# Optimization experiments

Hardware: AMD Instinct MI355X
Metric: run time of the kernel (lower is better)

The kernel has to match this reference:

```python
import jax, jax.numpy as jnp
import numpy as np

N, K, C, D4, HID, HEAD, DEPTH = 40000, 16, 128, 32, 512, 256, 4
EPS = 1e-5  # BatchNorm eps; eval mode with running_mean=0, running_var=1


def _bn(x, g, b):
    # eval-mode BatchNorm1d with fresh running stats (mean=0, var=1)
    return x * (g / np.sqrt(1.0 + EPS)) + b


def _mlp(x, w1, b1, w2, g, b):
    # Linear -> GELU -> Linear(no bias) -> BN
    return _bn(jax.nn.gelu(x @ w1 + b1) @ w2, g, b)


def _lfp(x, lxyz, knn, proj, coor, scale, g, b):
    # LFP: Linear(no bias) -> la_spse_a4 (neighbor gather + anisotropic spatial
    # positional encoding, one PE channel per 4 feature channels, max-pool over k) -> BN
    xp = x @ proj                                   # (N, C)
    xn = xp[knn]                                    # (N, K, C) irregular gather
    rel3 = (lxyz[knn] - lxyz[:, None])[..., :3]     # (N, K, 3)
    pe = jnp.einsum('nkc,cd->nkd', rel3, coor) * jnp.square(scale)  # (N, K, D4)
    out = jnp.max(xn.reshape(N, K, D4, 4) + pe[..., None], axis=1).reshape(N, C)
    return _bn(out, g, b)


def _knn_spse4(lxyz, feat, knn, m_sp, c, h):
    # knn_spse_4: squared anisotropic spatial distances (3 learned 4-d directions
    # per output channel, 12 params) + per-channel color (3) + height (1) weighted
    # squared diffs, averaged over k neighbors; caller takes sqrt.
    rel4 = lxyz[knn] - lxyz[:, None]                # (N, K, 4)
    relf = feat[knn] - feat[:, None]                # (N, K, 4) = color(3)+height(1)
    dirs = m_sp.reshape(3, 4, C)
    e = jnp.zeros((N, K, C), jnp.float32)
    for j in range(3):  # fixed small loop over 3 learned directions
        e = e + jnp.square(jnp.einsum('nkc,cd->nkd', rel4, dirs[j]))
    e = e + jnp.einsum('nki,id->nkd', jnp.square(relf[..., :3]), jnp.square(c))
    e = e + jnp.square(relf[..., 3:4]) * jnp.square(h)
    return jnp.sqrt(e.mean(axis=1))                 # (N, C)


def setup_inputs():
    key = jax.random.key(0)
    ks = jax.random.split(key, 32)
    rn = lambda i, s, sc=0.02: jax.random.normal(ks[i], s, jnp.float32) * sc
    gm = lambda i, s: 1.0 + jax.random.normal(ks[i], s, jnp.float32) * 0.1
    return {
        'x': rn(0, (N, 4), 1.0),
        'xyz': jax.random.uniform(ks[1], (N, 3), jnp.float32),
        'knn': jax.random.randint(ks[2], (N, K), 0, N, jnp.int32),
        'spse_m': rn(3, (12, C), 0.5),
        'spse_c': rn(4, (3, C), 0.5),
        'spse_h': rn(5, (C,), 0.5),
        'nbr_bn0_g': gm(6, (C,)), 'nbr_bn0_b': rn(7, (C,)),
        'nbr_w1': rn(8, (C, 2 * C)), 'nbr_b1': rn(9, (2 * C,)),
        'nbr_w2': rn(10, (2 * C, C)),
        'nbr_bn_g': gm(11, (C,)), 'nbr_bn_b': rn(12, (C,)),
        'lfp_proj': rn(13, (DEPTH, C, C)),
        'lfp_coor': rn(14, (DEPTH, 3, D4), 0.5),
        'lfp_scale': 0.1 + rn(15, (DEPTH, D4), 0.01),
        'lfp_bng': gm(16, (DEPTH, C)), 'lfp_bnb': rn(17, (DEPTH, C)),
        'mlp_w1': rn(18, (3, C, HID)), 'mlp_b1': rn(19, (3, HID)),
        'mlp_w2': rn(20, (3, HID, C)),
        'mlp_bng': gm(21, (3, C)), 'mlp_bnb': rn(22, (3, C)),
        'post_bn_g': gm(23, (C,)), 'post_bn_b': rn(24, (C,)),
        'post_w': rn(25, (C, HEAD)),
    }


def reference(x, xyz, knn, spse_m, spse_c, spse_h, nbr_bn0_g, nbr_bn0_b,
              nbr_w1, nbr_b1, nbr_w2, nbr_bn_g, nbr_bn_b,
              lfp_proj, lfp_coor, lfp_scale, lfp_bng, lfp_bnb,
              mlp_w1, mlp_b1, mlp_w2, mlp_bng, mlp_bnb,
              post_bn_g, post_bn_b, post_w):
    # Stage.forward, first==last stage, eval mode (no drop_path, no closs).
    lxyz = jnp.pad(xyz, ((0, 0), (0, 1)))  # cor_std = 1.0
    nbr = _knn_spse4(lxyz, x, knn, spse_m, spse_c, spse_h)
    nbr = _bn(nbr, nbr_bn0_g, nbr_bn0_b)
    nbr = jax.nn.gelu(nbr @ nbr_w1 + nbr_b1) @ nbr_w2   # nbr_proj
    h = _bn(nbr, nbr_bn_g, nbr_bn_b)                    # nbr_bn; x = nbr (first stage)
    # Block: residual MLP, then DEPTH LFPs with an MLP after every 2nd LFP
    h = h + _mlp(h, mlp_w1[0], mlp_b1[0], mlp_w2[0], mlp_bng[0], mlp_bnb[0])
    for i in range(DEPTH):
        h = h + _lfp(h, lxyz, knn, lfp_proj[i], lfp_coor[i], lfp_scale[i],
                     lfp_bng[i], lfp_bnb[i])
        if i % 2 == 1:
            j = i // 2 + 1
            h = h + _mlp(h, mlp_w1[j], mlp_b1[j], mlp_w2[j], mlp_bng[j], mlp_bnb[j])
    return _bn(h, post_bn_g, post_bn_b) @ post_w        # postproj -> (N, HEAD)
```

## Files before the change

kernel.cpp:

```cpp
#include <hip/hip_runtime.h>
#include <hip/hip_bf16.h>
#include <math.h>

#define NPTS 40000
#define KNB 16
#define CH 128

typedef unsigned short u16;
typedef __attribute__((ext_vector_type(8))) short bf16x8;
typedef __attribute__((ext_vector_type(4))) float f32x4;

__device__ __forceinline__ float gelu_f(float v) {
  const float u = 0.7978845608028654f * (v + 0.044715f * v * v * v);
  const float t = __builtin_amdgcn_exp2f(-2.8853900817779268f * u);
  return v * __builtin_amdgcn_rcpf(1.0f + t);
}

__device__ __forceinline__ float bnscale(float g) {
  return g * rsqrtf(1.0f + 1e-5f);
}

__device__ __forceinline__ u16 f2bf(float x) {
  union { __hip_bfloat16 b; u16 u; } cv;
  cv.b = __float2bfloat16(x);
  return cv.u;
}

__device__ __forceinline__ float bf2f(u16 u) {
  union { float f; unsigned int i; } cv;
  cv.i = ((unsigned int)u) << 16;
  return cv.f;
}

__device__ __forceinline__ void bf16split(float x, u16& hi, u16& lo) {
  hi = f2bf(x);
  lo = f2bf(x - bf2f(hi));
}

__device__ __forceinline__ void gl2lds(const u16* gp, u16* lp) {
  __builtin_amdgcn_global_load_lds(
      (const __attribute__((address_space(1))) void*)gp,
      (__attribute__((address_space(3))) void*)lp, 16, 0, 0);
}

__global__ __launch_bounds__(128) void spse_kernel(
    const float* __restrict__ x, const float* __restrict__ xyz,
    const int* __restrict__ knn, const float* __restrict__ sm,
    const float* __restrict__ sc, const float* __restrict__ sh,
    const float* __restrict__ g0, const float* __restrict__ b0,
    u16* __restrict__ oh, u16* __restrict__ ol) {
  const int n = blockIdx.x;
  const int c = threadIdx.x;
  __shared__ float sr[KNB][3];
  __shared__ float sf[KNB][4];
  if (c < KNB) {
    const int j = knn[n * KNB + c];
    sr[c][0] = xyz[j * 3 + 0] - xyz[n * 3 + 0];
    sr[c][1] = xyz[j * 3 + 1] - xyz[n * 3 + 1];
    sr[c][2] = xyz[j * 3 + 2] - xyz[n * 3 + 2];
    float f0 = x[j * 4 + 0] - x[n * 4 + 0];
    float f1 = x[j * 4 + 1] - x[n * 4 + 1];
    float f2 = x[j * 4 + 2] - x[n * 4 + 2];
    float f3 = x[j * 4 + 3] - x[n * 4 + 3];
    sf[c][0] = f0 * f0; sf[c][1] = f1 * f1;
    sf[c][2] = f2 * f2; sf[c][3] = f3 * f3;
  }
  __syncthreads();
  const float m0 = sm[c], m1 = sm[CH + c], m2 = sm[2 * CH + c];
  const float m4 = sm[4 * CH + c], m5 = sm[5 * CH + c], m6 = sm[6 * CH + c];
  const float m8 = sm[8 * CH + c], m9 = sm[9 * CH + c], m10 = sm[10 * CH + c];
  float c0 = sc[c];          c0 *= c0;
  float c1 = sc[CH + c];     c1 *= c1;
  float c2 = sc[2 * CH + c]; c2 *= c2;
  float h2 = sh[c];          h2 *= h2;
  float e = 0.0f;
#pragma unroll
  for (int k = 0; k < KNB; k++) {
    const float r0 = sr[k][0], r1 = sr[k][1], r2 = sr[k][2];
    const float d0 = fmaf(r2, m2, fmaf(r1, m1, r0 * m0));
    const float d1 = fmaf(r2, m6, fmaf(r1, m5, r0 * m4));
    const float d2 = fmaf(r2, m10, fmaf(r1, m9, r0 * m8));
    e = fmaf(d0, d0, e);
    e = fmaf(d1, d1, e);
    e = fmaf(d2, d2, e);
    e = fmaf(sf[k][0], c0, e);
    e = fmaf(sf[k][1], c1, e);
    e = fmaf(sf[k][2], c2, e);
    e = fmaf(sf[k][3], h2, e);
  }
  const float v = sqrtf(e * (1.0f / KNB)) * bnscale(g0[c]) + b0[c];
  u16 hi, lo; bf16split(v, hi, lo);
  const size_t idx = (size_t)n * CH + c;
  oh[idx] = hi; ol[idx] = lo;
}

__global__ __launch_bounds__(256) void lfp_kernel(
    const u16* __restrict__ xp, const int* __restrict__ knn,
    const float* __restrict__ xyz, const float* __restrict__ coor,
    const float* __restrict__ scale, const float* __restrict__ g,
    const float* __restrict__ b, u16* __restrict__ hh, u16* __restrict__ hl) {
  const int t = threadIdx.x;
  const int bid = blockIdx.x;
  __shared__ int si[16][KNB];
  __shared__ float sr[16][KNB][3];
  {
    const int pp = t >> 4, kk = t & 15;
    const int n = bid * 16 + pp;
    const int j = knn[n * KNB + kk];
    si[pp][kk] = j;
    sr[pp][kk][0] = xyz[j * 3 + 0] - xyz[n * 3 + 0];
    sr[pp][kk][1] = xyz[j * 3 + 1] - xyz[n * 3 + 1];
    sr[pp][kk][2] = xyz[j * 3 + 2] - xyz[n * 3 + 2];
  }
  __syncthreads();
  const int p = t >> 4, d8 = t & 15;
  const int n = bid * 16 + p;
  const float c0a = coor[d8 * 2],     c1a = coor[32 + d8 * 2],     c2a = coor[64 + d8 * 2];
  const float c0b = coor[d8 * 2 + 1], c1b = coor[32 + d8 * 2 + 1], c2b = coor[64 + d8 * 2 + 1];
  float s2a = scale[d8 * 2];     s2a *= s2a;
  float s2b = scale[d8 * 2 + 1]; s2b *= s2b;
  float a[8];
#pragma unroll
  for (int e = 0; e < 8; e++) a[e] = -3.0e38f;
#pragma unroll
  for (int k = 0; k < KNB; k++) {
    const int j = si[p][k];
    const float r0 = sr[p][k][0], r1 = sr[p][k][1], r2 = sr[p][k][2];
    const float pea = fmaf(r2, c2a, fmaf(r1, c1a, r0 * c0a)) * s2a;
    const float peb = fmaf(r2, c2b, fmaf(r1, c1b, r0 * c0b)) * s2b;
    const bf16x8 v = *(const bf16x8*)(xp + (size_t)j * CH + d8 * 8);
#pragma unroll
    for (int e = 0; e < 4; e++) a[e] = fmaxf(a[e], bf2f((u16)v[e]) + pea);
#pragma unroll
    for (int e = 4; e < 8; e++) a[e] = fmaxf(a[e], bf2f((u16)v[e]) + peb);
  }
  const size_t off = (size_t)n * CH + d8 * 8;
  union { u16 a[8]; uint4 v; } ih, il, oh, ol;
  ih.v = *(const uint4*)(hh + off);
  il.v = *(const uint4*)(hl + off);
#pragma unroll
  for (int e = 0; e < 8; e++) {
    const int c = d8 * 8 + e;
    const float nv = bf2f(ih.a[e]) + bf2f(il.a[e]) + a[e] * bnscale(g[c]) + b[c];
    u16 hi, lo; bf16split(nv, hi, lo);
    oh.a[e] = hi; ol.a[e] = lo;
  }
  *(uint4*)(hh + off) = oh.v;
  *(uint4*)(hl + off) = ol.v;
}

__global__ __launch_bounds__(256) void prep_weights(
    const float* __restrict__ nw1, const float* __restrict__ nw2,
    const float* __restrict__ mw1, const float* __restrict__ mw2,
    const float* __restrict__ lproj, const float* __restrict__ pw,
    const float* __restrict__ pg, u16* __restrict__ th, u16* __restrict__ tl) {
  const int idx = blockIdx.x * 256 + threadIdx.x;
  const float* src;
  int local, Kd, Nd, dst, swz;
  float scale = 1.0f;
  if (idx < 32768)        { src = nw1; local = idx;          Kd = 128; Nd = 256; dst = 0; swz = 0; }
  else if (idx < 65536)   { src = nw2; local = idx - 32768;  Kd = 256; Nd = 128; dst = 32768; swz = 1; }
  else if (idx < 262144)  { int j = (idx - 65536) >> 16;  local = (idx - 65536) & 65535;
                            src = mw1 + j * 65536; Kd = 128; Nd = 512; dst = 65536 + j * 65536; swz = 0; }
  else if (idx < 458752)  { int j = (idx - 262144) >> 16; local = (idx - 262144) & 65535;
                            src = mw2 + j * 65536; Kd = 512; Nd = 128; dst = 262144 + j * 65536; swz = 1; }
  else if (idx < 524288)  { int i = (idx - 458752) >> 14; local = (idx - 458752) & 16383;
                            src = lproj + i * 16384; Kd = 128; Nd = 128; dst = 458752 + i * 16384; swz = 0; }
  else if (idx < 557056)  { local = idx - 524288; src = pw; Kd = 128; Nd = 256; dst = 524288; swz = 0;
                            scale = bnscale(pg[local >> 8]); }
  else return;
  const int k = local / Nd, n = local % Nd;
  const float v = src[local] * scale;
  u16 hi, lo; bf16split(v, hi, lo);
  const int ks = swz ? ((k & ~63) | ((k & 63) ^ ((n & 7) << 3))) : k;
  const int o = dst + n * Kd + ks;
  th[o] = hi; tl[o] = lo;
}

__global__ __launch_bounds__(256) void fold_pb(const float* __restrict__ pw,
                                               const float* __restrict__ pb,
                                               float* __restrict__ fb) {
  const int t = threadIdx.x;
  float a = 0.0f;
  for (int k = 0; k < 128; k++) a = fmaf(pb[k], pw[k * 256 + t], a);
  fb[t] = a;
}

template <int EPI>
__global__ __launch_bounds__(256, 2) void k128_reg(
    const u16* __restrict__ Ahi, const u16* __restrict__ Alo,
    const u16* __restrict__ Wth, const u16* __restrict__ Wtl,
    const float* __restrict__ p0, u16* __restrict__ outu,
    float* __restrict__ outf, int ostride, int ntiles) {
  const int t = threadIdx.x, lane = t & 63, w = t >> 6;
  const int col0 = blockIdx.y * 128;
  const int wm0 = (w >> 1) * 32, wn0 = (w & 1) * 64;
  const int lc = lane & 15, lq = lane >> 4;
  const int lq8 = lq * 8, lq4 = lq * 4;

  bf16x8 wh[4][4], wl[4][4];
  float bv[4];
#pragma unroll
  for (int nf = 0; nf < 4; nf++) {
    const int nr = col0 + wn0 + nf * 16 + lc;
    const u16* wr = Wth + (size_t)nr * 128;
    const u16* wr2 = Wtl + (size_t)nr * 128;
#pragma unroll
    for (int ks = 0; ks < 4; ks++) {
      wh[nf][ks] = *(const bf16x8*)(wr + ks * 32 + lq8);
      wl[nf][ks] = *(const bf16x8*)(wr2 + ks * 32 + lq8);
    }
    bv[nf] = (EPI == 0) ? 0.0f : p0[nr];
  }

  const f32x4 zz = {0.0f, 0.0f, 0.0f, 0.0f};
  for (int tile = blockIdx.x; tile < ntiles; tile += gridDim.x) {
    const int row0 = tile * 64;
    f32x4 acc[2][4];
#pragma unroll
    for (int mf = 0; mf < 2; mf++)
#pragma unroll
      for (int nf = 0; nf < 4; nf++) acc[mf][nf] = zz;
#pragma unroll
    for (int ks = 0; ks < 4; ks++) {
      bf16x8 ah[2], al[2];
#pragma unroll
      for (int mf = 0; mf < 2; mf++) {
        const size_t ao = (size_t)(row0 + wm0 + mf * 16 + lc) * 128 + ks * 32 + lq8;
        ah[mf] = *(const bf16x8*)(Ahi + ao);
        al[mf] = *(const bf16x8*)(Alo + ao);
      }
#pragma unroll
      for (int mf = 0; mf < 2; mf++)
#pragma unroll
        for (int nf = 0; nf < 4; nf++) {
          acc[mf][nf] = __builtin_amdgcn_mfma_f32_16x16x32_bf16(ah[mf], wh[nf][ks], acc[mf][nf], 0, 0, 0);
          acc[mf][nf] = __builtin_amdgcn_mfma_f32_16x16x32_bf16(ah[mf], wl[nf][ks], acc[mf][nf], 0, 0, 0);
          acc[mf][nf] = __builtin_amdgcn_mfma_f32_16x16x32_bf16(al[mf], wh[nf][ks], acc[mf][nf], 0, 0, 0);
        }
    }
#pragma unroll
    for (int mf = 0; mf < 2; mf++)
#pragma unroll
      for (int q = 0; q < 4; q++) {
        const int r = row0 + wm0 + mf * 16 + lq4 + q;
#pragma unroll
        for (int nf = 0; nf < 4; nf++) {
          const int col = col0 + wn0 + nf * 16 + lc;
          const size_t off = (size_t)r * ostride + col;
          const float v = acc[mf][nf][q];
          if (EPI == 0)      outu[off] = f2bf(v);
          else if (EPI == 1) outu[off] = f2bf(gelu_f(v + bv[nf]));
          else               outf[off] = v + bv[nf];
        }
      }
  }
}

template <int K, bool RES>
__global__ __launch_bounds__(256, 3) void gemm_w2(
    const u16* __restrict__ A, const u16* __restrict__ Wth,
    const u16* __restrict__ Wtl, const float* __restrict__ g,
    const float* __restrict__ bb, u16* __restrict__ hh, u16* __restrict__ hl) {
  __shared__ __align__(16) u16 Ws[2][128 * 64];
  const int t = threadIdx.x, lane = t & 63, w = t >> 6;
  const int row0 = blockIdx.x * 64;
  const int wm0 = (w >> 1) * 32, wn0 = (w & 1) * 64;
  const int lc = lane & 15, lq = lane >> 4;
  const int lq8 = lq * 8, lq4 = lq * 4;

  const f32x4 zz = {0.0f, 0.0f, 0.0f, 0.0f};
  f32x4 acc[2][4];
#pragma unroll
  for (int mf = 0; mf < 2; mf++)
#pragma unroll
    for (int nf = 0; nf < 4; nf++) acc[mf][nf] = zz;

  auto stage_slab = [&](u16* lds, int kb) {
#pragma unroll
    for (int i = 0; i < 1024; i += 256) {
      const int wc0 = i + w * 64;
      const int c = wc0 + lane;
      gl2lds(Wth + (size_t)(c >> 3) * K + kb + (c & 7) * 8, lds + wc0 * 8);
    }
  };
  auto load_af = [&](bf16x8 (&dst)[2][2], int kb) {
#pragma unroll
    for (int mf = 0; mf < 2; mf++)
#pragma unroll
      for (int ks = 0; ks < 2; ks++)
        dst[mf][ks] = *(const bf16x8*)(A + (size_t)(row0 + wm0 + mf * 16 + lc) * K +
                                       kb + ks * 32 + lq8);
  };

  bf16x8 afc[2][2], afn[2][2];
  stage_slab(Ws[0], 0);
  load_af(afc, 0);
  __syncthreads();

  constexpr int NT = K / 64;
#pragma unroll 2
  for (int tt = 0; tt < NT; tt++) {
    const int cur = tt & 1;
    if (tt + 1 < NT) {
      stage_slab(Ws[cur ^ 1], (tt + 1) * 64);
      load_af(afn, (tt + 1) * 64);
    }
#pragma unroll
    for (int ks = 0; ks < 2; ks++) {
      bf16x8 whf[4], wlf[4];
#pragma unroll
      for (int nf = 0; nf < 4; nf++) {
        const int nr = wn0 + nf * 16 + lc;
        const int j = (ks * 32 + lq8) ^ ((nr & 7) << 3);
        whf[nf] = *(const bf16x8*)(Ws[cur] + nr * 64 + j);
        wlf[nf] = *(const bf16x8*)(Wtl + (size_t)nr * K + tt * 64 + j);
      }
#pragma unroll
      for (int mf = 0; mf < 2; mf++)
#pragma unroll
        for (int nf = 0; nf < 4; nf++) {
          acc[mf][nf] = __builtin_amdgcn_mfma_f32_16x16x32_bf16(afc[mf][ks], whf[nf], acc[mf][nf], 0, 0, 0);
          acc[mf][nf] = __builtin_amdgcn_mfma_f32_16x16x32_bf16(afc[mf][ks], wlf[nf], acc[mf][nf], 0, 0, 0);
        }
    }
    __syncthreads();
#pragma unroll
    for (int mf = 0; mf < 2; mf++)
#pragma unroll
      for (int ks = 0; ks < 2; ks++) afc[mf][ks] = afn[mf][ks];
  }

  float S0[4], S1[4];
#pragma unroll
  for (int nf = 0; nf < 4; nf++) {
    const int col = wn0 + nf * 16 + lc;
    S0[nf] = bnscale(g[col]);
    S1[nf] = bb[col];
  }
#pragma unroll
  for (int mf = 0; mf < 2; mf++)
#pragma unroll
    for (int q = 0; q < 4; q++) {
      const int r = row0 + wm0 + mf * 16 + lq4 + q;
#pragma unroll
      for (int nf = 0; nf < 4; nf++) {
        const int col = wn0 + nf * 16 + lc;
        const size_t off = (size_t)r * CH + col;
        float v = acc[mf][nf][q] * S0[nf] + S1[nf];
        if (RES) v += bf2f(hh[off]) + bf2f(hl[off]);
        u16 hi, lo; bf16split(v, hi, lo);
        hh[off] = hi; hl[off] = lo;
      }
    }
}

extern "C" void kernel_launch(void* const* d_in, const int* in_sizes, int n_in,
                              void* d_out, int out_size, void* d_ws, size_t ws_size,
                              hipStream_t stream) {
  const float* x    = (const float*)d_in[0];
  const float* xyz  = (const float*)d_in[1];
  const int*   knn  = (const int*)d_in[2];
  const float* sm   = (const float*)d_in[3];
  const float* scc  = (const float*)d_in[4];
  const float* shh  = (const float*)d_in[5];
  const float* bn0g = (const float*)d_in[6];
  const float* bn0b = (const float*)d_in[7];
  const float* nw1  = (const float*)d_in[8];
  const float* nb1  = (const float*)d_in[9];
  const float* nw2  = (const float*)d_in[10];
  const float* nbng = (const float*)d_in[11];
  const float* nbnb = (const float*)d_in[12];
  const float* lproj  = (const float*)d_in[13];
  const float* lcoor  = (const float*)d_in[14];
  const float* lscale = (const float*)d_in[15];
  const float* lbng   = (const float*)d_in[16];
  const float* lbnb   = (const float*)d_in[17];
  const float* mw1  = (const float*)d_in[18];
  const float* mb1  = (const float*)d_in[19];
  const float* mw2  = (const float*)d_in[20];
  const float* mbng = (const float*)d_in[21];
  const float* mbnb = (const float*)d_in[22];
  const float* pg   = (const float*)d_in[23];
  const float* pb   = (const float*)d_in[24];
  const float* pw   = (const float*)d_in[25];
  float* out = (float*)d_out;

  char* ws = (char*)d_ws;
  u16*   h_hi = (u16*)(ws + 0);
  u16*   h_lo = (u16*)(ws + 10240000);
  u16*   act  = (u16*)(ws + 20480000);
  u16*   xp   = (u16*)(ws + 20480000);
  u16*   Wh   = (u16*)(ws + 61440000);
  u16*   Wl   = (u16*)(ws + 62554112);
  float* fb   = (float*)(ws + 63668224);

  const u16* nw1t   = Wh + 0;
  const u16* nw2t   = Wh + 32768;
  const u16* mw1t   = Wh + 65536;
  const u16* mw2t   = Wh + 262144;
  const u16* lprojt = Wh + 458752;
  const u16* postt  = Wh + 524288;
  const u16* nw1tl   = Wl + 0;
  const u16* nw2tl   = Wl + 32768;
  const u16* mw1tl   = Wl + 65536;
  const u16* mw2tl   = Wl + 262144;
  const u16* lprojtl = Wl + 458752;
  const u16* posttl  = Wl + 524288;

  prep_weights<<<2176, 256, 0, stream>>>(nw1, nw2, mw1, mw2, lproj, pw, pg, Wh, Wl);
  fold_pb<<<1, 256, 0, stream>>>(pw, pb, fb);

  spse_kernel<<<NPTS, 128, 0, stream>>>(x, xyz, knn, sm, scc, shh, bn0g, bn0b, h_hi, h_lo);

  k128_reg<1><<<dim3(256, 2), 256, 0, stream>>>(h_hi, h_lo, nw1t, nw1tl, nb1,
                                                act, nullptr, 256, 625);
  gemm_w2<256, false><<<625, 256, 0, stream>>>(act, nw2t, nw2tl, nbng, nbnb, h_hi, h_lo);

  k128_reg<1><<<dim3(128, 4), 256, 0, stream>>>(h_hi, h_lo, mw1t, mw1tl, mb1,
                                                act, nullptr, 512, 625);
  gemm_w2<512, true><<<625, 256, 0, stream>>>(act, mw2t, mw2tl, mbng, mbnb, h_hi, h_lo);

  for (int i = 0; i < 4; i++) {
    k128_reg<0><<<dim3(625, 1), 256, 0, stream>>>(h_hi, h_lo, lprojt + i * 16384,
                                                  lprojtl + i * 16384, nullptr,
                                                  xp, nullptr, 128, 625);
    lfp_kernel<<<2500, 256, 0, stream>>>(xp, knn, xyz, lcoor + i * 96, lscale + i * 32,
                                         lbng + i * 128, lbnb + i * 128, h_hi, h_lo);
    if (i & 1) {
      const int j = i / 2 + 1;
      k128_reg<1><<<dim3(128, 4), 256, 0, stream>>>(h_hi, h_lo, mw1t + j * 65536,
                                                    mw1tl + j * 65536, mb1 + j * 512,
                                                    act, nullptr, 512, 625);
      gemm_w2<512, true><<<625, 256, 0, stream>>>(act, mw2t + j * 65536, mw2tl + j * 65536,
                                                  mbng + j * 128, mbnb + j * 128,
                                                  h_hi, h_lo);
    }
  }

  k128_reg<2><<<dim3(256, 2), 256, 0, stream>>>(h_hi, h_lo, postt, posttl, fb,
                                                nullptr, out, 256, 625);
}
```

Before: 497.2 us.

## Fuse MLP up- and down-projection GEMMs through LDS-resident hidden activations

Replaces the separate W1 GEMM (GELU epilogue writing a bf16 hidden buffer to global memory) and W2 GEMM with one kernel per MLP. Each 512-thread block computes a 64-row tile of the hidden activation, keeps it in a swizzled LDS buffer, then runs the second GEMM from LDS with the BN and residual epilogue. This removes the global write and read of the large (N x 512) intermediate and halves the launch count. In exchange, weights are read straight from global memory without LDS staging or double buffering. The 64 KB LDS footprint also allows only one block per CU, which limits latency hiding.

```diff
diff --git a/kernel.cpp b/kernel.cpp
--- a/kernel.cpp
+++ b/kernel.cpp
@@ -35,12 +35,6 @@
 __device__ __forceinline__ void bf16split(float x, u16& hi, u16& lo) {
   hi = f2bf(x);
   lo = f2bf(x - bf2f(hi));
-}
-
-__device__ __forceinline__ void gl2lds(const u16* gp, u16* lp) {
-  __builtin_amdgcn_global_load_lds(
-      (const __attribute__((address_space(1))) void*)gp,
-      (__attribute__((address_space(3))) void*)lp, 16, 0, 0);
 }
 
 __global__ __launch_bounds__(128) void spse_kernel(
@@ -156,24 +150,23 @@
     const float* __restrict__ pg, u16* __restrict__ th, u16* __restrict__ tl) {
   const int idx = blockIdx.x * 256 + threadIdx.x;
   const float* src;
-  int local, Kd, Nd, dst, swz;
+  int local, Kd, Nd, dst;
   float scale = 1.0f;
-  if (idx < 32768)        { src = nw1; local = idx;          Kd = 128; Nd = 256; dst = 0; swz = 0; }
-  else if (idx < 65536)   { src = nw2; local = idx - 32768;  Kd = 256; Nd = 128; dst = 32768; swz = 1; }
+  if (idx < 32768)        { src = nw1; local = idx;          Kd = 128; Nd = 256; dst = 0; }
+  else if (idx < 65536)   { src = nw2; local = idx - 32768;  Kd = 256; Nd = 128; dst = 32768; }
   else if (idx < 262144)  { int j = (idx - 65536) >> 16;  local = (idx - 65536) & 65535;
-                            src = mw1 + j * 65536; Kd = 128; Nd = 512; dst = 65536 + j * 65536; swz = 0; }
+                            src = mw1 + j * 65536; Kd = 128; Nd = 512; dst = 65536 + j * 65536; }
   else if (idx < 458752)  { int j = (idx - 262144) >> 16; local = (idx - 262144) & 65535;
-                            src = mw2 + j * 65536; Kd = 512; Nd = 128; dst = 262144 + j * 65536; swz = 1; }
+                            src = mw2 + j * 65536; Kd = 512; Nd = 128; dst = 262144 + j * 65536; }
   else if (idx < 524288)  { int i = (idx - 458752) >> 14; local = (idx - 458752) & 16383;
-                            src = lproj + i * 16384; Kd = 128; Nd = 128; dst = 458752 + i * 16384; swz = 0; }
-  else if (idx < 557056)  { local = idx - 524288; src = pw; Kd = 128; Nd = 256; dst = 524288; swz = 0;
+                            src = lproj + i * 16384; Kd = 128; Nd = 128; dst = 458752 + i * 16384; }
+  else if (idx < 557056)  { local = idx - 524288; src = pw; Kd = 128; Nd = 256; dst = 524288;
                             scale = bnscale(pg[local >> 8]); }
   else return;
   const int k = local / Nd, n = local % Nd;
   const float v = src[local] * scale;
   u16 hi, lo; bf16split(v, hi, lo);
-  const int ks = swz ? ((k & ~63) | ((k & 63) ^ ((n & 7) << 3))) : k;
-  const int o = dst + n * Kd + ks;
+  const int o = dst + n * Kd + k;
   th[o] = hi; tl[o] = lo;
 }
 
@@ -249,92 +242,115 @@
           const int col = col0 + wn0 + nf * 16 + lc;
           const size_t off = (size_t)r * ostride + col;
           const float v = acc[mf][nf][q];
-          if (EPI == 0)      outu[off] = f2bf(v);
-          else if (EPI == 1) outu[off] = f2bf(gelu_f(v + bv[nf]));
-          else               outf[off] = v + bv[nf];
+          if (EPI == 0) outu[off] = f2bf(v);
+          else          outf[off] = v + bv[nf];
         }
       }
   }
 }
 
-template <int K, bool RES>
-__global__ __launch_bounds__(256, 3) void gemm_w2(
-    const u16* __restrict__ A, const u16* __restrict__ Wth,
-    const u16* __restrict__ Wtl, const float* __restrict__ g,
+template <int HID, bool RES>
+__global__ __launch_bounds__(512, 1) void mlp_fused(
+    const u16* __restrict__ Ahi, const u16* __restrict__ Alo,
+    const u16* __restrict__ W1t, const u16* __restrict__ W1tl,
+    const u16* __restrict__ W2t, const u16* __restrict__ W2tl,
+    const float* __restrict__ b1, const float* __restrict__ g,
     const float* __restrict__ bb, u16* __restrict__ hh, u16* __restrict__ hl) {
-  __shared__ __align__(16) u16 Ws[2][128 * 64];
+  constexpr int HID8 = HID / 8;
+  constexpr int NF1 = HID8 / 16;
+  constexpr int NKS2 = HID / 32;
+  __shared__ __align__(16) u16 act[64 * HID];
   const int t = threadIdx.x, lane = t & 63, w = t >> 6;
   const int row0 = blockIdx.x * 64;
-  const int wm0 = (w >> 1) * 32, wn0 = (w & 1) * 64;
   const int lc = lane & 15, lq = lane >> 4;
   const int lq8 = lq * 8, lq4 = lq * 4;
+  const int cw0 = w * HID8;
 
   const f32x4 zz = {0.0f, 0.0f, 0.0f, 0.0f};
-  f32x4 acc[2][4];
+  f32x4 acc1[4][NF1];
+#pragma unroll
+  for (int mf = 0; mf < 4; mf++)
+#pragma unroll
+    for (int nf = 0; nf < NF1; nf++) acc1[mf][nf] = zz;
+
+#pragma unroll
+  for (int ks = 0; ks < 4; ks++) {
+    bf16x8 ah[4], al[4];
+#pragma unroll
+    for (int mf = 0; mf < 4; mf++) {
+      const size_t ao = (size_t)(row0 + mf * 16 + lc) * 128 + ks * 32 + lq8;
+      ah[mf] = *(const bf16x8*)(Ahi + ao);
+      al[mf] = *(const bf16x8*)(Alo + ao);
+    }
+    bf16x8 w1h[NF1], w1l[NF1];
+#pragma unroll
+    for (int nf = 0; nf < NF1; nf++) {
+      const size_t wo = (size_t)(cw0 + nf * 16 + lc) * 128 + ks * 32 + lq8;
+      w1h[nf] = *(const bf16x8*)(W1t + wo);
+      w1l[nf] = *(const bf16x8*)(W1tl + wo);
+    }
+#pragma unroll
+    for (int mf = 0; mf < 4; mf++)
+#pragma unroll
+      for (int nf = 0; nf < NF1; nf++) {
+        acc1[mf][nf] = __builtin_amdgcn_mfma_f32_16x16x32_bf16(ah[mf], w1h[nf], acc1[mf][nf], 0, 0, 0);
+        acc1[mf][nf] = __builtin_amdgcn_mfma_f32_16x16x32_bf16(ah[mf], w1l[nf], acc1[mf][nf], 0, 0, 0);
+        acc1[mf][nf] = __builtin_amdgcn_mfma_f32_16x16x32_bf16(al[mf], w1h[nf], acc1[mf][nf], 0, 0, 0);
+      }
+  }
+  float b1v[NF1];
+#pragma unroll
+  for (int nf = 0; nf < NF1; nf++) b1v[nf] = b1[cw0 + nf * 16 + lc];
+#pragma unroll
+  for (int mf = 0; mf < 4; mf++)
+#pragma unroll
+    for (int nf = 0; nf < NF1; nf++)
+#pragma unroll
+      for (int q = 0; q < 4; q++) {
+        const int row = mf * 16 + lq4 + q;
+        const int col = cw0 + nf * 16 + lc;
+        const int cs = (col & ~63) | ((col & 63) ^ ((row & 7) << 3));
+        act[row * HID + cs] = f2bf(gelu_f(acc1[mf][nf][q] + b1v[nf]));
+      }
+  __syncthreads();
+
+  const int wr = w >> 2, wc = w & 3;
+  f32x4 acc[2][2];
 #pragma unroll
   for (int mf = 0; mf < 2; mf++)
 #pragma unroll
-    for (int nf = 0; nf < 4; nf++) acc[mf][nf] = zz;
-
-  auto stage_slab = [&](u16* lds, int kb) {
-#pragma unroll
-    for (int i = 0; i < 1024; i += 256) {
-      const int wc0 = i + w * 64;
-      const int c = wc0 + lane;
-      gl2lds(Wth + (size_t)(c >> 3) * K + kb + (c & 7) * 8, lds + wc0 * 8);
-    }
-  };
-  auto load_af = [&](bf16x8 (&dst)[2][2], int kb) {
+    for (int nf = 0; nf < 2; nf++) acc[mf][nf] = zz;
+
+#pragma unroll
+  for (int ks = 0; ks < NKS2; ks++) {
+    bf16x8 af[2];
+#pragma unroll
+    for (int mf = 0; mf < 2; mf++) {
+      const int r = wr * 32 + mf * 16 + lc;
+      const int cb = ks * 32 + lq8;
+      const int cs = (cb & ~63) | ((cb & 63) ^ ((r & 7) << 3));
+      af[mf] = *(const bf16x8*)(act + r * HID + cs);
+    }
+    bf16x8 w2h[2], w2l[2];
+#pragma unroll
+    for (int nf = 0; nf < 2; nf++) {
+      const size_t wo = (size_t)(wc * 32 + nf * 16 + lc) * HID + ks * 32 + lq8;
+      w2h[nf] = *(const bf16x8*)(W2t + wo);
+      w2l[nf] = *(const bf16x8*)(W2tl + wo);
+    }
 #pragma unroll
     for (int mf = 0; mf < 2; mf++)
 #pragma unroll
-      for (int ks = 0; ks < 2; ks++)
-        dst[mf][ks] = *(const bf16x8*)(A + (size_t)(row0 + wm0 + mf * 16 + lc) * K +
-                                       kb + ks * 32 + lq8);
-  };
-
-  bf16x8 afc[2][2], afn[2][2];
-  stage_slab(Ws[0], 0);
-  load_af(afc, 0);
-  __syncthreads();
-
-  constexpr int NT = K / 64;
-#pragma unroll 2
-  for (int tt = 0; tt < NT; tt++) {
-    const int cur = tt & 1;
-    if (tt + 1 < NT) {
-      stage_slab(Ws[cur ^ 1], (tt + 1) * 64);
-      load_af(afn, (tt + 1) * 64);
-    }
-#pragma unroll
-    for (int ks = 0; ks < 2; ks++) {
-      bf16x8 whf[4], wlf[4];
-#pragma unroll
-      for (int nf = 0; nf < 4; nf++) {
-        const int nr = wn0 + nf * 16 + lc;
-        const int j = (ks * 32 + lq8) ^ ((nr & 7) << 3);
-        whf[nf] = *(const bf16x8*)(Ws[cur] + nr * 64 + j);
-        wlf[nf] = *(const bf16x8*)(Wtl + (size_t)nr * K + tt * 64 + j);
-      }
-#pragma unroll
-      for (int mf = 0; mf < 2; mf++)
-#pragma unroll
-        for (int nf = 0; nf < 4; nf++) {
-          acc[mf][nf] = __builtin_amdgcn_mfma_f32_16x16x32_bf16(afc[mf][ks], whf[nf], acc[mf][nf], 0, 0, 0);
-          acc[mf][nf] = __builtin_amdgcn_mfma_f32_16x16x32_bf16(afc[mf][ks], wlf[nf], acc[mf][nf], 0, 0, 0);
-        }
-    }
-    __syncthreads();
-#pragma unroll
-    for (int mf = 0; mf < 2; mf++)
-#pragma unroll
-      for (int ks = 0; ks < 2; ks++) afc[mf][ks] = afn[mf][ks];
-  }
-
-  float S0[4], S1[4];
-#pragma unroll
-  for (int nf = 0; nf < 4; nf++) {
-    const int col = wn0 + nf * 16 + lc;
+      for (int nf = 0; nf < 2; nf++) {
+        acc[mf][nf] = __builtin_amdgcn_mfma_f32_16x16x32_bf16(af[mf], w2h[nf], acc[mf][nf], 0, 0, 0);
+        acc[mf][nf] = __builtin_amdgcn_mfma_f32_16x16x32_bf16(af[mf], w2l[nf], acc[mf][nf], 0, 0, 0);
+      }
+  }
+
+  float S0[2], S1[2];
+#pragma unroll
+  for (int nf = 0; nf < 2; nf++) {
+    const int col = wc * 32 + nf * 16 + lc;
     S0[nf] = bnscale(g[col]);
     S1[nf] = bb[col];
   }
@@ -342,10 +358,10 @@
   for (int mf = 0; mf < 2; mf++)
 #pragma unroll
     for (int q = 0; q < 4; q++) {
-      const int r = row0 + wm0 + mf * 16 + lq4 + q;
-#pragma unroll
-      for (int nf = 0; nf < 4; nf++) {
-        const int col = wn0 + nf * 16 + lc;
+      const int r = row0 + wr * 32 + mf * 16 + lq4 + q;
+#pragma unroll
+      for (int nf = 0; nf < 2; nf++) {
+        const int col = wc * 32 + nf * 16 + lc;
         const size_t off = (size_t)r * CH + col;
         float v = acc[mf][nf][q] * S0[nf] + S1[nf];
         if (RES) v += bf2f(hh[off]) + bf2f(hl[off]);
@@ -389,7 +405,6 @@
   char* ws = (char*)d_ws;
   u16*   h_hi = (u16*)(ws + 0);
   u16*   h_lo = (u16*)(ws + 10240000);
-  u16*   act  = (u16*)(ws + 20480000);
   u16*   xp   = (u16*)(ws + 20480000);
   u16*   Wh   = (u16*)(ws + 61440000);
   u16*   Wl   = (u16*)(ws + 62554112);
@@ -413,13 +428,10 @@
 
   spse_kernel<<<NPTS, 128, 0, stream>>>(x, xyz, knn, sm, scc, shh, bn0g, bn0b, h_hi, h_lo);
 
-  k128_reg<1><<<dim3(256, 2), 256, 0, stream>>>(h_hi, h_lo, nw1t, nw1tl, nb1,
-                                                act, nullptr, 256, 625);
-  gemm_w2<256, false><<<625, 256, 0, stream>>>(act, nw2t, nw2tl, nbng, nbnb, h_hi, h_lo);
-
-  k128_reg<1><<<dim3(128, 4), 256, 0, stream>>>(h_hi, h_lo, mw1t, mw1tl, mb1,
-                                                act, nullptr, 512, 625);
-  gemm_w2<512, true><<<625, 256, 0, stream>>>(act, mw2t, mw2tl, mbng, mbnb, h_hi, h_lo);
+  mlp_fused<256, false><<<625, 512, 0, stream>>>(
+      h_hi, h_lo, nw1t, nw1tl, nw2t, nw2tl, nb1, nbng, nbnb, h_hi, h_lo);
+  mlp_fused<512, true><<<625, 512, 0, stream>>>(
+      h_hi, h_lo, mw1t, mw1tl, mw2t, mw2tl, mb1, mbng, mbnb, h_hi, h_lo);
 
   for (int i = 0; i < 4; i++) {
     k128_reg<0><<<dim3(625, 1), 256, 0, stream>>>(h_hi, h_lo, lprojt + i * 16384,
@@ -429,12 +441,9 @@
                                          lbng + i * 128, lbnb + i * 128, h_hi, h_lo);
     if (i & 1) {
       const int j = i / 2 + 1;
-      k128_reg<1><<<dim3(128, 4), 256, 0, stream>>>(h_hi, h_lo, mw1t + j * 65536,
-                                                    mw1tl + j * 65536, mb1 + j * 512,
-                                                    act, nullptr, 512, 625);
-      gemm_w2<512, true><<<625, 256, 0, stream>>>(act, mw2t + j * 65536, mw2tl + j * 65536,
-                                                  mbng + j * 128, mbnb + j * 128,
-                                                  h_hi, h_lo);
+      mlp_fused<512, true><<<625, 512, 0, stream>>>(
+          h_hi, h_lo, mw1t + j * 65536, mw1tl + j * 65536, mw2t + j * 65536,
+          mw2tl + j * 65536, mb1 + j * 512, mbng + j * 128, mbnb + j * 128, h_hi, h_lo);
     }
   }
 
```

New measurement: 619.9 us. 24.7% more time.

## Drop activation-low split in hidden GEMMs and simplify W2 GEMM to direct global loads

Applied to the files above, without the earlier changes.

The k128_reg GEMMs gain an NSPLIT template parameter. Every layer except the final post-projection drops the activation-low term, so each of those GEMMs issues 2 MFMAs per fragment instead of 3 and skips loading the Alo tile. The gemm_w2 kernel loses its LDS double-buffered weight staging and swizzle and now reads the weight hi and lo fragments straight from global memory, with occupancy bound lowered from 3 to 2. This cuts matrix-core work and removes LDS and sync overhead, at the cost of lower precision in the hidden layers and more global or L2 traffic for weights.

```diff
diff --git a/kernel.cpp b/kernel.cpp
--- a/kernel.cpp
+++ b/kernel.cpp
@@ -35,12 +35,6 @@
 __device__ __forceinline__ void bf16split(float x, u16& hi, u16& lo) {
   hi = f2bf(x);
   lo = f2bf(x - bf2f(hi));
-}
-
-__device__ __forceinline__ void gl2lds(const u16* gp, u16* lp) {
-  __builtin_amdgcn_global_load_lds(
-      (const __attribute__((address_space(1))) void*)gp,
-      (__attribute__((address_space(3))) void*)lp, 16, 0, 0);
 }
 
 __global__ __launch_bounds__(128) void spse_kernel(
@@ -156,24 +150,23 @@
     const float* __restrict__ pg, u16* __restrict__ th, u16* __restrict__ tl) {
   const int idx = blockIdx.x * 256 + threadIdx.x;
   const float* src;
-  int local, Kd, Nd, dst, swz;
+  int local, Kd, Nd, dst;
   float scale = 1.0f;
-  if (idx < 32768)        { src = nw1; local = idx;          Kd = 128; Nd = 256; dst = 0; swz = 0; }
-  else if (idx < 65536)   { src = nw2; local = idx - 32768;  Kd = 256; Nd = 128; dst = 32768; swz = 1; }
+  if (idx < 32768)        { src = nw1; local = idx;          Kd = 128; Nd = 256; dst = 0; }
+  else if (idx < 65536)   { src = nw2; local = idx - 32768;  Kd = 256; Nd = 128; dst = 32768; }
   else if (idx < 262144)  { int j = (idx - 65536) >> 16;  local = (idx - 65536) & 65535;
-                            src = mw1 + j * 65536; Kd = 128; Nd = 512; dst = 65536 + j * 65536; swz = 0; }
+                            src = mw1 + j * 65536; Kd = 128; Nd = 512; dst = 65536 + j * 65536; }
   else if (idx < 458752)  { int j = (idx - 262144) >> 16; local = (idx - 262144) & 65535;
-                            src = mw2 + j * 65536; Kd = 512; Nd = 128; dst = 262144 + j * 65536; swz = 1; }
+                            src = mw2 + j * 65536; Kd = 512; Nd = 128; dst = 262144 + j * 65536; }
   else if (idx < 524288)  { int i = (idx - 458752) >> 14; local = (idx - 458752) & 16383;
-                            src = lproj + i * 16384; Kd = 128; Nd = 128; dst = 458752 + i * 16384; swz = 0; }
-  else if (idx < 557056)  { local = idx - 524288; src = pw; Kd = 128; Nd = 256; dst = 524288; swz = 0;
+                            src = lproj + i * 16384; Kd = 128; Nd = 128; dst = 458752 + i * 16384; }
+  else if (idx < 557056)  { local = idx - 524288; src = pw; Kd = 128; Nd = 256; dst = 524288;
                             scale = bnscale(pg[local >> 8]); }
   else return;
   const int k = local / Nd, n = local % Nd;
   const float v = src[local] * scale;
   u16 hi, lo; bf16split(v, hi, lo);
-  const int ks = swz ? ((k & ~63) | ((k & 63) ^ ((n & 7) << 3))) : k;
-  const int o = dst + n * Kd + ks;
+  const int o = dst + n * Kd + k;
   th[o] = hi; tl[o] = lo;
 }
 
@@ -186,7 +179,7 @@
   fb[t] = a;
 }
 
-template <int EPI>
+template <int EPI, int NSPLIT>
 __global__ __launch_bounds__(256, 2) void k128_reg(
     const u16* __restrict__ Ahi, const u16* __restrict__ Alo,
     const u16* __restrict__ Wth, const u16* __restrict__ Wtl,
@@ -228,7 +221,7 @@
       for (int mf = 0; mf < 2; mf++) {
         const size_t ao = (size_t)(row0 + wm0 + mf * 16 + lc) * 128 + ks * 32 + lq8;
         ah[mf] = *(const bf16x8*)(Ahi + ao);
-        al[mf] = *(const bf16x8*)(Alo + ao);
+        if (NSPLIT == 3) al[mf] = *(const bf16x8*)(Alo + ao);
       }
 #pragma unroll
       for (int mf = 0; mf < 2; mf++)
@@ -236,7 +229,8 @@
         for (int nf = 0; nf < 4; nf++) {
           acc[mf][nf] = __builtin_amdgcn_mfma_f32_16x16x32_bf16(ah[mf], wh[nf][ks], acc[mf][nf], 0, 0, 0);
           acc[mf][nf] = __builtin_amdgcn_mfma_f32_16x16x32_bf16(ah[mf], wl[nf][ks], acc[mf][nf], 0, 0, 0);
-          acc[mf][nf] = __builtin_amdgcn_mfma_f32_16x16x32_bf16(al[mf], wh[nf][ks], acc[mf][nf], 0, 0, 0);
+          if (NSPLIT == 3)
+            acc[mf][nf] = __builtin_amdgcn_mfma_f32_16x16x32_bf16(al[mf], wh[nf][ks], acc[mf][nf], 0, 0, 0);
         }
     }
 #pragma unroll
@@ -258,11 +252,10 @@
 }
 
 template <int K, bool RES>
-__global__ __launch_bounds__(256, 3) void gemm_w2(
+__global__ __launch_bounds__(256, 2) void gemm_w2(
     const u16* __restrict__ A, const u16* __restrict__ Wth,
     const u16* __restrict__ Wtl, const float* __restrict__ g,
     const float* __restrict__ bb, u16* __restrict__ hh, u16* __restrict__ hl) {
-  __shared__ __align__(16) u16 Ws[2][128 * 64];
   const int t = threadIdx.x, lane = t & 63, w = t >> 6;
   const int row0 = blockIdx.x * 64;
   const int wm0 = (w >> 1) * 32, wn0 = (w & 1) * 64;
@@ -276,59 +269,28 @@
 #pragma unroll
     for (int nf = 0; nf < 4; nf++) acc[mf][nf] = zz;
 
-  auto stage_slab = [&](u16* lds, int kb) {
-#pragma unroll
-    for (int i = 0; i < 1024; i += 256) {
-      const int wc0 = i + w * 64;
-      const int c = wc0 + lane;
-      gl2lds(Wth + (size_t)(c >> 3) * K + kb + (c & 7) * 8, lds + wc0 * 8);
-    }
-  };
-  auto load_af = [&](bf16x8 (&dst)[2][2], int kb) {
-#pragma unroll
-    for (int mf = 0; mf < 2; mf++)
-#pragma unroll
-      for (int ks = 0; ks < 2; ks++)
-        dst[mf][ks] = *(const bf16x8*)(A + (size_t)(row0 + wm0 + mf * 16 + lc) * K +
-                                       kb + ks * 32 + lq8);
-  };
-
-  bf16x8 afc[2][2], afn[2][2];
-  stage_slab(Ws[0], 0);
-  load_af(afc, 0);
-  __syncthreads();
-
-  constexpr int NT = K / 64;
-#pragma unroll 2
-  for (int tt = 0; tt < NT; tt++) {
-    const int cur = tt & 1;
-    if (tt + 1 < NT) {
-      stage_slab(Ws[cur ^ 1], (tt + 1) * 64);
-      load_af(afn, (tt + 1) * 64);
-    }
-#pragma unroll
-    for (int ks = 0; ks < 2; ks++) {
-      bf16x8 whf[4], wlf[4];
-#pragma unroll
-      for (int nf = 0; nf < 4; nf++) {
-        const int nr = wn0 + nf * 16 + lc;
-        const int j = (ks * 32 + lq8) ^ ((nr & 7) << 3);
-        whf[nf] = *(const bf16x8*)(Ws[cur] + nr * 64 + j);
-        wlf[nf] = *(const bf16x8*)(Wtl + (size_t)nr * K + tt * 64 + j);
-      }
-#pragma unroll
-      for (int mf = 0; mf < 2; mf++)
-#pragma unroll
-        for (int nf = 0; nf < 4; nf++) {
-          acc[mf][nf] = __builtin_amdgcn_mfma_f32_16x16x32_bf16(afc[mf][ks], whf[nf], acc[mf][nf], 0, 0, 0);
-          acc[mf][nf] = __builtin_amdgcn_mfma_f32_16x16x32_bf16(afc[mf][ks], wlf[nf], acc[mf][nf], 0, 0, 0);
-        }
-    }
-    __syncthreads();
-#pragma unroll
-    for (int mf = 0; mf < 2; mf++)
-#pragma unroll
-      for (int ks = 0; ks < 2; ks++) afc[mf][ks] = afn[mf][ks];
+  const u16* arow0 = A + (size_t)(row0 + wm0 + lc) * K;
+  const u16* arow1 = A + (size_t)(row0 + wm0 + 16 + lc) * K;
+
+#pragma unroll
+  for (int ks = 0; ks < K / 32; ks++) {
+    const int e = ks * 32 + lq8;
+    const bf16x8 af0 = *(const bf16x8*)(arow0 + e);
+    const bf16x8 af1 = *(const bf16x8*)(arow1 + e);
+    bf16x8 whf[4], wlf[4];
+#pragma unroll
+    for (int nf = 0; nf < 4; nf++) {
+      const size_t wo = (size_t)(wn0 + nf * 16 + lc) * K + e;
+      whf[nf] = *(const bf16x8*)(Wth + wo);
+      wlf[nf] = *(const bf16x8*)(Wtl + wo);
+    }
+#pragma unroll
+    for (int nf = 0; nf < 4; nf++) {
+      acc[0][nf] = __builtin_amdgcn_mfma_f32_16x16x32_bf16(af0, whf[nf], acc[0][nf], 0, 0, 0);
+      acc[0][nf] = __builtin_amdgcn_mfma_f32_16x16x32_bf16(af0, wlf[nf], acc[0][nf], 0, 0, 0);
+      acc[1][nf] = __builtin_amdgcn_mfma_f32_16x16x32_bf16(af1, whf[nf], acc[1][nf], 0, 0, 0);
+      acc[1][nf] = __builtin_amdgcn_mfma_f32_16x16x32_bf16(af1, wlf[nf], acc[1][nf], 0, 0, 0);
+    }
   }
 
   float S0[4], S1[4];
@@ -413,31 +375,31 @@
 
   spse_kernel<<<NPTS, 128, 0, stream>>>(x, xyz, knn, sm, scc, shh, bn0g, bn0b, h_hi, h_lo);
 
-  k128_reg<1><<<dim3(256, 2), 256, 0, stream>>>(h_hi, h_lo, nw1t, nw1tl, nb1,
-                                                act, nullptr, 256, 625);
+  k128_reg<1, 2><<<dim3(256, 2), 256, 0, stream>>>(h_hi, h_lo, nw1t, nw1tl, nb1,
+                                                   act, nullptr, 256, 625);
   gemm_w2<256, false><<<625, 256, 0, stream>>>(act, nw2t, nw2tl, nbng, nbnb, h_hi, h_lo);
 
-  k128_reg<1><<<dim3(128, 4), 256, 0, stream>>>(h_hi, h_lo, mw1t, mw1tl, mb1,
-                                                act, nullptr, 512, 625);
+  k128_reg<1, 2><<<dim3(128, 4), 256, 0, stream>>>(h_hi, h_lo, mw1t, mw1tl, mb1,
+                                                   act, nullptr, 512, 625);
   gemm_w2<512, true><<<625, 256, 0, stream>>>(act, mw2t, mw2tl, mbng, mbnb, h_hi, h_lo);
 
   for (int i = 0; i < 4; i++) {
-    k128_reg<0><<<dim3(625, 1), 256, 0, stream>>>(h_hi, h_lo, lprojt + i * 16384,
-                                                  lprojtl + i * 16384, nullptr,
-                                                  xp, nullptr, 128, 625);
+    k128_reg<0, 2><<<dim3(625, 1), 256, 0, stream>>>(h_hi, h_lo, lprojt + i * 16384,
+                                                     lprojtl + i * 16384, nullptr,
+                                                     xp, nullptr, 128, 625);
     lfp_kernel<<<2500, 256, 0, stream>>>(xp, knn, xyz, lcoor + i * 96, lscale + i * 32,
                                          lbng + i * 128, lbnb + i * 128, h_hi, h_lo);
     if (i & 1) {
       const int j = i / 2 + 1;
-      k128_reg<1><<<dim3(128, 4), 256, 0, stream>>>(h_hi, h_lo, mw1t + j * 65536,
-                                                    mw1tl + j * 65536, mb1 + j * 512,
-                                                    act, nullptr, 512, 625);
+      k128_reg<1, 2><<<dim3(128, 4), 256, 0, stream>>>(h_hi, h_lo, mw1t + j * 65536,
+                                                       mw1tl + j * 65536, mb1 + j * 512,
+                                                       act, nullptr, 512, 625);
       gemm_w2<512, true><<<625, 256, 0, stream>>>(act, mw2t + j * 65536, mw2tl + j * 65536,
                                                   mbng + j * 128, mbnb + j * 128,
                                                   h_hi, h_lo);
     }
   }
 
-  k128_reg<2><<<dim3(256, 2), 256, 0, stream>>>(h_hi, h_lo, postt, posttl, fb,
-                                                nullptr, out, 256, 625);
-}
+  k128_reg<2, 3><<<dim3(256, 2), 256, 0, stream>>>(h_hi, h_lo, postt, posttl, fb,
+                                                   nullptr, out, 256, 625);
+}
```

Result: slower. 573.0 us (+15.2%).
